# Optimization experiments

Hardware: AMD Instinct MI355X
Metric: run time of the kernel (lower is better)

Reference implementation:

```python
import jax, jax.numpy as jnp
import numpy as np

NUM_HEADS = 12
HIDDEN = 768
HEAD_DIM = HIDDEN // NUM_HEADS  # 64
B, S = 2, 2048


def setup_inputs() -> dict:
    key = jax.random.key(0)
    ks = jax.random.split(key, 8)
    inp = {
        "hidden_states": jax.random.normal(ks[0], (B, S, HIDDEN), dtype=jnp.float32),
        "attention_mask": jnp.zeros((B, 1, 1, S), dtype=jnp.float32),
        "Wq": jax.random.normal(ks[1], (HIDDEN, HIDDEN), dtype=jnp.float32) * 0.02,
        "bq": jnp.zeros((HIDDEN,), dtype=jnp.float32),
        "Wk": jax.random.normal(ks[2], (HIDDEN, HIDDEN), dtype=jnp.float32) * 0.02,
        "bk": jnp.zeros((HIDDEN,), dtype=jnp.float32),
        "Wv": jax.random.normal(ks[3], (HIDDEN, HIDDEN), dtype=jnp.float32) * 0.02,
        "bv": jnp.zeros((HIDDEN,), dtype=jnp.float32),
    }
    return inp


def _split_heads(x):
    # [B, S, H*d] -> [B, H, S, d]
    b, s, _ = x.shape
    return x.reshape(b, s, NUM_HEADS, HEAD_DIM).transpose(0, 2, 1, 3)


def reference(hidden_states, attention_mask, Wq, bq, Wk, bk, Wv, bv):
    # Q/K/V projections (nn.Linear: x @ W.T + b; W generated square so direct matmul is equivalent math)
    q = _split_heads(hidden_states @ Wq + bq)  # [B,H,S,d]
    k = _split_heads(hidden_states @ Wk + bk)
    v = _split_heads(hidden_states @ Wv + bv)

    scale = 1.0 / np.sqrt(HEAD_DIM).astype(np.float32)
    scores = jnp.einsum("bhqd,bhkd->bhqk", q, k) * scale  # [B,H,S,S]
    scores = scores + attention_mask  # additive mask, broadcast [B,1,1,S]
    probs = jax.nn.softmax(scores, axis=-1)
    # dropout prob = 0.0 -> identity (eval mode)
    ctx = jnp.einsum("bhqk,bhkd->bhqd", probs, v)  # [B,H,S,d]
    ctx = ctx.transpose(0, 2, 1, 3).reshape(hidden_states.shape[0], hidden_states.shape[1], HIDDEN)
    return ctx
```

## Files before the change

kernel.cpp:

```cpp
#include <hip/hip_runtime.h>

#define S_LEN 2048
#define HID   768
#define NH    12
#define HD    64
#define BATCH 2
#define GK    768
#define L2E   1.44269504088896340736f
#define QSCL  (0.125f * L2E)

typedef __attribute__((ext_vector_type(8))) short bf16x8;
typedef __attribute__((ext_vector_type(4))) float f32x4;
typedef __attribute__((ext_vector_type(4))) short s16x4;
typedef __attribute__((ext_vector_type(8))) short s16x8;

__device__ __forceinline__ unsigned short f2bf(float f) {
    union { float f; unsigned int u; } v; v.f = f;
    unsigned int r = v.u + 0x7fffu + ((v.u >> 16) & 1u);
    return (unsigned short)(r >> 16);
}
__device__ __forceinline__ unsigned short f2bf_hu(float f) {
    union { float f; unsigned int u; } v; v.f = f;
    return (unsigned short)((v.u + 0x8000u) >> 16);
}

__device__ __forceinline__ unsigned int cvtpk(float a, float b) {
    unsigned int r;
    asm("v_cvt_pk_bf16_f32 %0, %1, %2" : "=v"(r) : "v"(a), "v"(b));
    return r;
}

#define GLL16(gp, lp) __builtin_amdgcn_global_load_lds( \
    (const __attribute__((address_space(1))) unsigned int*)(gp), \
    (__attribute__((address_space(3))) unsigned int*)(lp), 16, 0, 0)


__global__ __launch_bounds__(256) void prep_kernel(
    const float* __restrict__ X, const float* __restrict__ Wq,
    const float* __restrict__ Wk, const float* __restrict__ Wv,
    unsigned short* __restrict__ Xb, unsigned short* __restrict__ Wt) {
    __shared__ float T[32][33];
    int bid = blockIdx.x;
    if (bid < 3072) {
        int id = bid * 256 + threadIdx.x;
        float4 v = ((const float4*)X)[id];
        s16x4 o; o[0] = (short)f2bf(v.x); o[1] = (short)f2bf(v.y);
        o[2] = (short)f2bf(v.z); o[3] = (short)f2bf(v.w);
        ((s16x4*)Xb)[id] = o;
        return;
    }
    int t2 = bid - 3072;
    int mat = t2 / 576, t = t2 % 576;
    int tk = t / 24, tn = t % 24;
    const float* W = (mat == 0) ? Wq : (mat == 1) ? Wk : Wv;
    const float scl = (mat == 0) ? QSCL : 1.0f;
    int r  = threadIdx.x >> 3;
    int c4 = (threadIdx.x & 7) * 4;
    float4 v = *(const float4*)&W[(size_t)(tk*32 + r) * GK + tn*32 + c4];
    T[c4+0][r] = v.x; T[c4+1][r] = v.y; T[c4+2][r] = v.z; T[c4+3][r] = v.w;
    __syncthreads();
    s16x4 o;
    o[0] = (short)f2bf(T[r][c4+0] * scl); o[1] = (short)f2bf(T[r][c4+1] * scl);
    o[2] = (short)f2bf(T[r][c4+2] * scl); o[3] = (short)f2bf(T[r][c4+3] * scl);
    *(s16x4*)&Wt[(size_t)(mat*768 + tn*32 + r) * GK + tk*32 + c4] = o;
}

__global__ __launch_bounds__(256) void gemm_qkv(
    const unsigned short* __restrict__ Xb, const unsigned short* __restrict__ Wt,
    const float* __restrict__ bq, const float* __restrict__ bk,
    const float* __restrict__ bv,
    unsigned short* __restrict__ qb, unsigned short* __restrict__ kb,
    unsigned short* __restrict__ vb) {
    __shared__ __align__(16) unsigned short As[128][64];
    __shared__ __align__(16) unsigned short Bs[64][64];

    const int tid = threadIdx.x;
    const int bm = blockIdx.y * 128;
    const int bn = blockIdx.x * 64;
    const int w = tid >> 6, l = tid & 63, quad = l >> 4, lq = l & 15;
    const int wx = w & 1, wy = w >> 1;

    const int srow = l >> 3, schunk = ((l & 7) ^ (l >> 3)) * 8;
    const unsigned short* aga = Xb + (size_t)(bm + w*32 + srow) * GK + schunk;
    const unsigned short* bga = Wt + (size_t)(bn + w*16 + srow) * GK + schunk;

    const int c0 = ((quad)     ^ (lq & 7)) * 8;
    const int c1 = ((4 + quad) ^ (lq & 7)) * 8;

    f32x4 zero = {0.f, 0.f, 0.f, 0.f};
    f32x4 acc[4][2];
#pragma unroll
    for (int mi = 0; mi < 4; mi++)
#pragma unroll
        for (int ni = 0; ni < 2; ni++) acc[mi][ni] = zero;

    for (int k0 = 0; k0 < GK; k0 += 64) {
        __syncthreads();
#pragma unroll
        for (int i = 0; i < 4; i++)
            GLL16(aga + k0 + i*8*GK, &As[w*32 + i*8][0]);
#pragma unroll
        for (int i = 0; i < 2; i++)
            GLL16(bga + k0 + i*8*GK, &Bs[w*16 + i*8][0]);
        __syncthreads();
#pragma unroll
        for (int kh = 0; kh < 2; kh++) {
            const int cc = kh ? c1 : c0;
            bf16x8 a[4], b[2];
#pragma unroll
            for (int mi = 0; mi < 4; mi++)
                a[mi] = *(const bf16x8*)&As[wy*64 + mi*16 + lq][cc];
#pragma unroll
            for (int ni = 0; ni < 2; ni++)
                b[ni] = *(const bf16x8*)&Bs[wx*32 + ni*16 + lq][cc];
#pragma unroll
            for (int mi = 0; mi < 4; mi++)
#pragma unroll
                for (int ni = 0; ni < 2; ni++)
                    acc[mi][ni] = __builtin_amdgcn_mfma_f32_16x16x32_bf16(
                        a[mi], b[ni], acc[mi][ni], 0, 0, 0);
        }
    }

    const int mat = bn / 768;
    const float* bias = (mat == 0) ? bq : (mat == 1) ? bk : bv;
    const float bscl = (mat == 0) ? QSCL : 1.0f;
    const int nbase = bn % 768;
#pragma unroll
    for (int ni = 0; ni < 2; ni++) {
        int hn = nbase + wx*32 + ni*16 + lq;
        float bval = bias[hn] * bscl;
        int h = hn >> 6, d = hn & 63;
#pragma unroll
        for (int mi = 0; mi < 4; mi++) {
            int m0 = bm + wy*64 + mi*16 + quad*4;
            int b_ = m0 >> 11, s0 = m0 & 2047;
            if (mat != 1) {
                unsigned short* outp = (mat == 0) ? qb : vb;
                s16x4 pk;
#pragma unroll
                for (int r = 0; r < 4; r++) pk[r] = (short)f2bf_hu(acc[mi][ni][r] + bval);
                *(s16x4*)&outp[((size_t)((b_*NH + h) * HD + d)) * S_LEN + s0] = pk;
            } else {
                size_t base = ((size_t)((b_*NH + h) * S_LEN + s0)) * HD + d;
#pragma unroll
                for (int r = 0; r < 4; r++)
                    kb[base + (size_t)r * HD] = f2bf_hu(acc[mi][ni][r] + bval);
            }
        }
    }
}

__global__ __launch_bounds__(256) void attn_kernel(
    const unsigned short* __restrict__ Qtg, const unsigned short* __restrict__ Kg,
    const unsigned short* __restrict__ Vtg, const float* __restrict__ maskg,
    float* __restrict__ out) {
    __shared__ __align__(16) unsigned short Ks[2][64][64];
    __shared__ __align__(16) unsigned short Vt[2][64][64];
    __shared__ __align__(16) unsigned short Ps[4][16][64];
    __shared__ __align__(16) float mkL[S_LEN];

    const int tid = threadIdx.x;
    const int w = tid >> 6, l = tid & 63, quad = l >> 4, lq = l & 15;

    const int wgid = blockIdx.y * gridDim.x + blockIdx.x;
    const int virt = (wgid & 7) * 96 + (wgid >> 3);
    const int bh = virt >> 5;
    const int q0 = (virt & 31) * 64;
    const int bi = bh / NH, hi = bh % NH;
    const unsigned short* Kh = Kg + (size_t)bh * S_LEN * HD;
    const unsigned short* Vh = Vtg + (size_t)bh * HD * S_LEN;

    bf16x8 a0, a1;
    {
        const unsigned short* Qt = Qtg + (size_t)bh * HD * S_LEN + (q0 + w*16 + lq);
#pragma unroll
        for (int j = 0; j < 8; j++) {
            a0[j] = (short)Qt[(size_t)(quad*8 + j) * S_LEN];
            a1[j] = (short)Qt[(size_t)(quad*8 + j + 32) * S_LEN];
        }
    }

    {
        const float4* mb4 = (const float4*)(maskg + (size_t)bi * S_LEN);
#pragma unroll
        for (int i = 0; i < 2; i++) {
            int idx = i * 256 + tid;
            float4 v = mb4[idx];
            float4 sv; sv.x = v.x*L2E; sv.y = v.y*L2E; sv.z = v.z*L2E; sv.w = v.w*L2E;
            ((float4*)mkL)[idx] = sv;
        }
    }

    bf16x8 ones;
#pragma unroll
    for (int i = 0; i < 8; i++) ones[i] = (short)0x3F80;

    const int srow = l >> 3, schunk = ((l & 7) ^ (l >> 3)) * 8;
    const unsigned short* kga = Kh + (size_t)(w*16 + srow) * HD + schunk;
    const unsigned short* vga = Vh + (size_t)(w*16 + srow) * S_LEN + schunk;

    const int c0 = ((quad)     ^ (lq & 7)) * 8;
    const int c1 = ((4 + quad) ^ (lq & 7)) * 8;
    const int pqh = quad >> 1;
    const int po  = (quad & 1) * 4;
    const int pe  = lq & 7;

    f32x4 zero = {0.f, 0.f, 0.f, 0.f};
    f32x4 o[4], lsum = zero;
#pragma unroll
    for (int ng = 0; ng < 4; ng++) o[ng] = zero;

    auto stage = [&](int buf, int kt) {
#pragma unroll
        for (int i = 0; i < 2; i++) {
            GLL16(kga + (size_t)kt*64*HD + i*8*HD, &Ks[buf][w*16 + i*8][0]);
            GLL16(vga + kt*64 + (size_t)i*8*S_LEN, &Vt[buf][w*16 + i*8][0]);
        }
    };

    auto compute = [&](int buf, int kt) {
        const int kk = kt * 64;

        f32x4 st[4];
#pragma unroll
        for (int g = 0; g < 4; g++) {
            bf16x8 b0 = *(const bf16x8*)&Ks[buf][g*16 + lq][c0];
            bf16x8 b1 = *(const bf16x8*)&Ks[buf][g*16 + lq][c1];
            f32x4 z = __builtin_amdgcn_mfma_f32_16x16x32_bf16(b0, a0, zero, 0, 0, 0);
            st[g]   = __builtin_amdgcn_mfma_f32_16x16x32_bf16(b1, a1, z,    0, 0, 0);
        }

#pragma unroll
        for (int g = 0; g < 4; g++) {
            const f32x4 mmg = *(const f32x4*)&mkL[kk + g*16 + quad*4];
            float p0 = exp2f(st[g][0] + mmg[0]);
            float p1 = exp2f(st[g][1] + mmg[1]);
            float p2 = exp2f(st[g][2] + mmg[2]);
            float p3 = exp2f(st[g][3] + mmg[3]);
            uint2 pr;
            pr.x = cvtpk(p0, p1);
            pr.y = cvtpk(p2, p3);
            *(uint2*)&Ps[w][lq][((g*2 + pqh) ^ pe) * 8 + po] = pr;
        }

        bf16x8 pa0 = *(const bf16x8*)&Ps[w][lq][c0];
        bf16x8 pa1 = *(const bf16x8*)&Ps[w][lq][c1];

        lsum = __builtin_amdgcn_mfma_f32_16x16x32_bf16(pa0, ones, lsum, 0, 0, 0);
        lsum = __builtin_amdgcn_mfma_f32_16x16x32_bf16(pa1, ones, lsum, 0, 0, 0);

#pragma unroll
        for (int ng = 0; ng < 4; ng++) {
            bf16x8 v0 = *(const bf16x8*)&Vt[buf][ng*16 + lq][c0];
            bf16x8 v1 = *(const bf16x8*)&Vt[buf][ng*16 + lq][c1];
            f32x4 t = __builtin_amdgcn_mfma_f32_16x16x32_bf16(pa0, v0, o[ng], 0, 0, 0);
            o[ng]   = __builtin_amdgcn_mfma_f32_16x16x32_bf16(pa1, v1, t,     0, 0, 0);
        }
    };

    stage(0, 0);
    __syncthreads();

    for (int kt = 0; kt < S_LEN / 64; kt += 2) {
        stage(1, kt + 1);
        compute(0, kt);
        __syncthreads();
        if (kt + 2 < S_LEN / 64) stage(0, kt + 2);
        compute(1, kt + 1);
        __syncthreads();
    }

#pragma unroll
    for (int r = 0; r < 4; r++) {
        const float inv = 1.0f / lsum[r];
        const int row = q0 + w*16 + quad*4 + r;
#pragma unroll
        for (int ng = 0; ng < 4; ng++)
            out[((size_t)(bi * S_LEN + row)) * HID + hi*HD + ng*16 + lq] = o[ng][r] * inv;
    }
}

extern "C" void kernel_launch(void* const* d_in, const int* in_sizes, int n_in,
                              void* d_out, int out_size, void* d_ws, size_t ws_size,
                              hipStream_t stream) {
    const float* X    = (const float*)d_in[0];
    const float* mask = (const float*)d_in[1];
    const float* Wq   = (const float*)d_in[2];
    const float* bq   = (const float*)d_in[3];
    const float* Wk   = (const float*)d_in[4];
    const float* bk   = (const float*)d_in[5];
    const float* Wv   = (const float*)d_in[6];
    const float* bv   = (const float*)d_in[7];
    float* out = (float*)d_out;

    const size_t per = (size_t)BATCH * NH * S_LEN * HD;
    unsigned short* qb = (unsigned short*)d_ws;
    unsigned short* kb = qb + per;
    unsigned short* vb = kb + per;
    unsigned short* xb = vb + per;
    unsigned short* wt = xb + (size_t)4096 * GK;

    prep_kernel<<<4800, 256, 0, stream>>>(X, Wq, Wk, Wv, xb, wt);

    dim3 ggrid(2304 / 64, 4096 / 128);
    gemm_qkv<<<ggrid, 256, 0, stream>>>(xb, wt, bq, bk, bv, qb, kb, vb);

    dim3 agrid(S_LEN / 64, BATCH * NH);
    attn_kernel<<<agrid, 256, 0, stream>>>(qb, kb, vb, mask, out);
}
```

Before: 160.3 us.

## Enlarge QKV GEMM tiles, precompute mask, fold mask into MFMA accumulator

```diff
diff --git a/kernel.cpp b/kernel.cpp
--- a/kernel.cpp
+++ b/kernel.cpp
@@ -30,6 +30,16 @@
     return r;
 }
 
+#if __has_builtin(__builtin_amdgcn_exp2f)
+#define EXP2(x) __builtin_amdgcn_exp2f(x)
+#else
+__device__ __forceinline__ float EXP2(float x) {
+    float r;
+    asm volatile("v_exp_f32 %0, %1\n\ts_nop 0" : "=v"(r) : "v"(x));
+    return r;
+}
+#endif
+
 #define GLL16(gp, lp) __builtin_amdgcn_global_load_lds( \
     (const __attribute__((address_space(1))) unsigned int*)(gp), \
     (__attribute__((address_space(3))) unsigned int*)(lp), 16, 0, 0)
@@ -38,9 +48,18 @@
 __global__ __launch_bounds__(256) void prep_kernel(
     const float* __restrict__ X, const float* __restrict__ Wq,
     const float* __restrict__ Wk, const float* __restrict__ Wv,
-    unsigned short* __restrict__ Xb, unsigned short* __restrict__ Wt) {
+    const float* __restrict__ maskg,
+    unsigned short* __restrict__ Xb, unsigned short* __restrict__ Wt,
+    float* __restrict__ wsm) {
     __shared__ float T[32][33];
     int bid = blockIdx.x;
+    if (bid >= 4800) {
+        int idx = (bid - 4800) * 256 + threadIdx.x;
+        float4 v = ((const float4*)maskg)[idx];
+        float4 s; s.x = v.x*L2E; s.y = v.y*L2E; s.z = v.z*L2E; s.w = v.w*L2E;
+        ((float4*)wsm)[idx] = s;
+        return;
+    }
     if (bid < 3072) {
         int id = bid * 256 + threadIdx.x;
         float4 v = ((const float4*)X)[id];
@@ -72,51 +91,52 @@
     unsigned short* __restrict__ qb, unsigned short* __restrict__ kb,
     unsigned short* __restrict__ vb) {
     __shared__ __align__(16) unsigned short As[128][64];
-    __shared__ __align__(16) unsigned short Bs[64][64];
+    __shared__ __align__(16) unsigned short Bs[128][64];
 
     const int tid = threadIdx.x;
-    const int bm = blockIdx.y * 128;
-    const int bn = blockIdx.x * 64;
+    const int wgid = blockIdx.y * gridDim.x + blockIdx.x;
+    const int virt = (wgid & 7) * 72 + (wgid >> 3);
+    const int bm = (virt / 18) * 128;
+    const int bn = (virt % 18) * 128;
     const int w = tid >> 6, l = tid & 63, quad = l >> 4, lq = l & 15;
     const int wx = w & 1, wy = w >> 1;
 
     const int srow = l >> 3, schunk = ((l & 7) ^ (l >> 3)) * 8;
     const unsigned short* aga = Xb + (size_t)(bm + w*32 + srow) * GK + schunk;
-    const unsigned short* bga = Wt + (size_t)(bn + w*16 + srow) * GK + schunk;
+    const unsigned short* bga = Wt + (size_t)(bn + w*32 + srow) * GK + schunk;
 
     const int c0 = ((quad)     ^ (lq & 7)) * 8;
     const int c1 = ((4 + quad) ^ (lq & 7)) * 8;
 
     f32x4 zero = {0.f, 0.f, 0.f, 0.f};
-    f32x4 acc[4][2];
+    f32x4 acc[4][4];
 #pragma unroll
     for (int mi = 0; mi < 4; mi++)
 #pragma unroll
-        for (int ni = 0; ni < 2; ni++) acc[mi][ni] = zero;
+        for (int ni = 0; ni < 4; ni++) acc[mi][ni] = zero;
 
     for (int k0 = 0; k0 < GK; k0 += 64) {
         __syncthreads();
 #pragma unroll
-        for (int i = 0; i < 4; i++)
+        for (int i = 0; i < 4; i++) {
             GLL16(aga + k0 + i*8*GK, &As[w*32 + i*8][0]);
-#pragma unroll
-        for (int i = 0; i < 2; i++)
-            GLL16(bga + k0 + i*8*GK, &Bs[w*16 + i*8][0]);
+            GLL16(bga + k0 + i*8*GK, &Bs[w*32 + i*8][0]);
+        }
         __syncthreads();
 #pragma unroll
         for (int kh = 0; kh < 2; kh++) {
             const int cc = kh ? c1 : c0;
-            bf16x8 a[4], b[2];
+            bf16x8 a[4], b[4];
 #pragma unroll
             for (int mi = 0; mi < 4; mi++)
                 a[mi] = *(const bf16x8*)&As[wy*64 + mi*16 + lq][cc];
 #pragma unroll
-            for (int ni = 0; ni < 2; ni++)
-                b[ni] = *(const bf16x8*)&Bs[wx*32 + ni*16 + lq][cc];
+            for (int ni = 0; ni < 4; ni++)
+                b[ni] = *(const bf16x8*)&Bs[wx*64 + ni*16 + lq][cc];
 #pragma unroll
             for (int mi = 0; mi < 4; mi++)
 #pragma unroll
-                for (int ni = 0; ni < 2; ni++)
+                for (int ni = 0; ni < 4; ni++)
                     acc[mi][ni] = __builtin_amdgcn_mfma_f32_16x16x32_bf16(
                         a[mi], b[ni], acc[mi][ni], 0, 0, 0);
         }
@@ -127,8 +147,8 @@
     const float bscl = (mat == 0) ? QSCL : 1.0f;
     const int nbase = bn % 768;
 #pragma unroll
-    for (int ni = 0; ni < 2; ni++) {
-        int hn = nbase + wx*32 + ni*16 + lq;
+    for (int ni = 0; ni < 4; ni++) {
+        int hn = nbase + wx*64 + ni*16 + lq;
         float bval = bias[hn] * bscl;
         int h = hn >> 6, d = hn & 63;
 #pragma unroll
@@ -151,14 +171,13 @@
     }
 }
 
-__global__ __launch_bounds__(256) void attn_kernel(
+__global__ __launch_bounds__(256, 4) void attn_kernel(
     const unsigned short* __restrict__ Qtg, const unsigned short* __restrict__ Kg,
-    const unsigned short* __restrict__ Vtg, const float* __restrict__ maskg,
+    const unsigned short* __restrict__ Vtg, const float* __restrict__ wsm,
     float* __restrict__ out) {
     __shared__ __align__(16) unsigned short Ks[2][64][64];
     __shared__ __align__(16) unsigned short Vt[2][64][64];
     __shared__ __align__(16) unsigned short Ps[4][16][64];
-    __shared__ __align__(16) float mkL[S_LEN];
 
     const int tid = threadIdx.x;
     const int w = tid >> 6, l = tid & 63, quad = l >> 4, lq = l & 15;
@@ -170,6 +189,7 @@
     const int bi = bh / NH, hi = bh % NH;
     const unsigned short* Kh = Kg + (size_t)bh * S_LEN * HD;
     const unsigned short* Vh = Vtg + (size_t)bh * HD * S_LEN;
+    const float* wsmb = wsm + (size_t)bi * S_LEN;
 
     bf16x8 a0, a1;
     {
@@ -178,17 +198,6 @@
         for (int j = 0; j < 8; j++) {
             a0[j] = (short)Qt[(size_t)(quad*8 + j) * S_LEN];
             a1[j] = (short)Qt[(size_t)(quad*8 + j + 32) * S_LEN];
-        }
-    }
-
-    {
-        const float4* mb4 = (const float4*)(maskg + (size_t)bi * S_LEN);
-#pragma unroll
-        for (int i = 0; i < 2; i++) {
-            int idx = i * 256 + tid;
-            float4 v = mb4[idx];
-            float4 sv; sv.x = v.x*L2E; sv.y = v.y*L2E; sv.z = v.z*L2E; sv.w = v.w*L2E;
-            ((float4*)mkL)[idx] = sv;
         }
     }
 
@@ -219,25 +228,28 @@
         }
     };
 
-    auto compute = [&](int buf, int kt) {
-        const int kk = kt * 64;
-
+    auto ldm = [&](f32x4* dst, int kt) {
+#pragma unroll
+        for (int g = 0; g < 4; g++)
+            dst[g] = *(const f32x4*)&wsmb[kt*64 + g*16 + quad*4];
+    };
+
+    auto compute = [&](int buf, const f32x4* mk) {
         f32x4 st[4];
 #pragma unroll
         for (int g = 0; g < 4; g++) {
             bf16x8 b0 = *(const bf16x8*)&Ks[buf][g*16 + lq][c0];
             bf16x8 b1 = *(const bf16x8*)&Ks[buf][g*16 + lq][c1];
-            f32x4 z = __builtin_amdgcn_mfma_f32_16x16x32_bf16(b0, a0, zero, 0, 0, 0);
-            st[g]   = __builtin_amdgcn_mfma_f32_16x16x32_bf16(b1, a1, z,    0, 0, 0);
+            f32x4 z = __builtin_amdgcn_mfma_f32_16x16x32_bf16(b0, a0, mk[g], 0, 0, 0);
+            st[g]   = __builtin_amdgcn_mfma_f32_16x16x32_bf16(b1, a1, z,     0, 0, 0);
         }
 
 #pragma unroll
         for (int g = 0; g < 4; g++) {
-            const f32x4 mmg = *(const f32x4*)&mkL[kk + g*16 + quad*4];
-            float p0 = exp2f(st[g][0] + mmg[0]);
-            float p1 = exp2f(st[g][1] + mmg[1]);
-            float p2 = exp2f(st[g][2] + mmg[2]);
-            float p3 = exp2f(st[g][3] + mmg[3]);
+            float p0 = EXP2(st[g][0]);
+            float p1 = EXP2(st[g][1]);
+            float p2 = EXP2(st[g][2]);
+            float p3 = EXP2(st[g][3]);
             uint2 pr;
             pr.x = cvtpk(p0, p1);
             pr.y = cvtpk(p2, p3);
@@ -259,15 +271,17 @@
         }
     };
 
+    f32x4 mkA[4], mkB[4];
+    ldm(mkA, 0);
     stage(0, 0);
     __syncthreads();
 
     for (int kt = 0; kt < S_LEN / 64; kt += 2) {
-        stage(1, kt + 1);
-        compute(0, kt);
+        stage(1, kt + 1); ldm(mkB, kt + 1);
+        compute(0, mkA);
         __syncthreads();
-        if (kt + 2 < S_LEN / 64) stage(0, kt + 2);
-        compute(1, kt + 1);
+        if (kt + 2 < S_LEN / 64) { stage(0, kt + 2); ldm(mkA, kt + 2); }
+        compute(1, mkB);
         __syncthreads();
     }
 
@@ -300,12 +314,13 @@
     unsigned short* vb = kb + per;
     unsigned short* xb = vb + per;
     unsigned short* wt = xb + (size_t)4096 * GK;
-
-    prep_kernel<<<4800, 256, 0, stream>>>(X, Wq, Wk, Wv, xb, wt);
-
-    dim3 ggrid(2304 / 64, 4096 / 128);
+    float* wsm = (float*)(wt + (size_t)2304 * GK);
+
+    prep_kernel<<<4804, 256, 0, stream>>>(X, Wq, Wk, Wv, mask, xb, wt, wsm);
+
+    dim3 ggrid(18, 32);
     gemm_qkv<<<ggrid, 256, 0, stream>>>(xb, wt, bq, bk, bv, qb, kb, vb);
 
     dim3 agrid(S_LEN / 64, BATCH * NH);
-    attn_kernel<<<agrid, 256, 0, stream>>>(qb, kb, vb, mask, out);
-}
+    attn_kernel<<<agrid, 256, 0, stream>>>(qb, kb, vb, wsm, out);
+}
```

New measurement: 155.7 us. 1.03x faster.
